# Performance work log

Hardware: AMD Instinct MI355X
Metric: run time of the kernel (lower is better)

## Reference

```python
import jax, jax.numpy as jnp
import numpy as np

HEADS = 8
DK = 64            # key_size == size_per_head
NEIGHBORS = 3
KSIZE = 1 + 2 * NEIGHBORS  # 7 (rate=1)


def setup_inputs() -> dict:
    key = jax.random.key(0)
    k1, k2, k3, k4 = jax.random.split(key, 4)
    B, HW, S, D = 2, 64, 256, 512
    inputs = jax.random.normal(k1, (B, HW, S, D), dtype=jnp.float32)
    pos_bias = jax.random.normal(k2, (HEADS, S, KSIZE), dtype=jnp.float32)
    W_qkv = jax.random.normal(k3, (D, 3 * HEADS * DK), dtype=jnp.float32) * 0.02
    W_out = jax.random.normal(k4, (HEADS * DK, D), dtype=jnp.float32) * 0.02
    return {"inputs": inputs, "pos_bias": pos_bias, "W_qkv": W_qkv, "W_out": W_out}


def reference(inputs, pos_bias, W_qkv, W_out):
    B, HW, S, D = inputs.shape
    # qkv projection (no bias), split into q, k, v
    qkv = inputs @ W_qkv                                   # [B,HW,S,3*H*DK]
    q, k, v = jnp.split(qkv, 3, axis=-1)
    q = (q / jnp.sqrt(jnp.float32(DK))).reshape(B, HW, S, HEADS, DK)
    k = k.reshape(B, HW, S, HEADS, DK)
    v = v.reshape(B, HW, S, HEADS, DK)

    # zero-pad keys/values along seq (faithful to F.pad with value=0)
    pad = NEIGHBORS
    kp = jnp.pad(k, ((0, 0), (0, 0), (pad, pad), (0, 0), (0, 0)))
    vp = jnp.pad(v, ((0, 0), (0, 0), (pad, pad), (0, 0), (0, 0)))

    # sliding-window gather: window w for query i covers padded positions i..i+KSIZE-1
    idx = jnp.arange(S)[:, None] + jnp.arange(KSIZE)[None, :]  # [S,KSIZE]
    kw = kp[:, :, idx]                                         # [B,HW,S,KSIZE,H,DK]
    vw = vp[:, :, idx]                                         # [B,HW,S,KSIZE,H,DK]

    # scores over the window
    attn = jnp.einsum('bnshd,bnswhd->bnswh', q, kw)            # [B,HW,S,KSIZE,H]
    # additive positional bias: [H,S,KSIZE] -> [S,KSIZE,H] broadcast
    attn = attn + jnp.transpose(pos_bias, (1, 2, 0))[None, None]
    attn = jax.nn.softmax(attn, axis=-2)                       # softmax over window dim

    out = jnp.einsum('bnswh,bnswhd->bnshd', attn, vw)          # [B,HW,S,H,DK]
    out = out.reshape(B, HW, S, HEADS * DK)
    return out @ W_out
```

## Files before the change

kernel.cpp:

```cpp
#include <hip/hip_runtime.h>
#include <hip/hip_bf16.h>
#include <cstdint>


typedef __bf16 bf16x8 __attribute__((ext_vector_type(8)));
typedef float f32x4 __attribute__((ext_vector_type(4)));

__device__ __forceinline__ uint16_t f2bf(float f) {
    uint32_t u = __builtin_bit_cast(uint32_t, f);
    return (uint16_t)((u + 0x7fffu + ((u >> 16) & 1u)) >> 16);
}
__device__ __forceinline__ float bflo(uint32_t u) { return __builtin_bit_cast(float, u << 16); }
__device__ __forceinline__ float bfhi(uint32_t u) { return __builtin_bit_cast(float, u & 0xffff0000u); }

__device__ __forceinline__ void unpack8(uint4 v, float* f) {
    f[0] = bflo(v.x); f[1] = bfhi(v.x);
    f[2] = bflo(v.y); f[3] = bfhi(v.y);
    f[4] = bflo(v.z); f[5] = bfhi(v.z);
    f[6] = bflo(v.w); f[7] = bfhi(v.w);
}
__device__ __forceinline__ uint32_t pack2(float a, float b) {
    return (uint32_t)f2bf(a) | ((uint32_t)f2bf(b) << 16);
}

#define GLOAD_LDS16(gp, lp)                                                        \
    __builtin_amdgcn_global_load_lds((const __attribute__((address_space(1))) void*)(gp), \
                                     (__attribute__((address_space(3))) void*)(lp), 16, 0, 0)

__device__ __forceinline__ bf16x8 ds_read16(const uint16_t* p) {
    bf16x8 r;
    asm volatile("ds_read_b128 %0, %1"
                 : "=v"(r)
                 : "v"((const __attribute__((address_space(3))) void*)p));
    return r;
}

__global__ void cvt_f32_bf16(const float* __restrict__ in, uint16_t* __restrict__ out, int n8) {
    int i = blockIdx.x * 256 + threadIdx.x;
    if (i >= n8) return;
    const float4* p = (const float4*)in + (size_t)i * 2;
    float4 a = p[0], b = p[1];
    uint4 o;
    o.x = pack2(a.x, a.y);
    o.y = pack2(a.z, a.w);
    o.z = pack2(b.x, b.y);
    o.w = pack2(b.z, b.w);
    *((uint4*)out + i) = o;
}

__global__ void transpose_cvt(const float* __restrict__ in, uint16_t* __restrict__ out,
                              int R, int C) {
    int idx = blockIdx.x * 256 + threadIdx.x;
    if (idx >= R * C) return;
    int r = idx / C;
    int c = idx - r * C;
    out[(size_t)c * R + r] = f2bf(in[idx]);
}

template <bool F32OUT>
__global__ __launch_bounds__(512, 2)
void gemm256(const uint16_t* __restrict__ A, const uint16_t* __restrict__ BT,
             void* __restrict__ Cout, int M, int N, int K) {
    __shared__ __align__(16) uint16_t lds[65536];

    const int tid  = threadIdx.x;
    const int lane = tid & 63;
    const int wv   = tid >> 6;
    const int r    = lane & 15;
    const int quad = lane >> 4;
    const int wr   = wv >> 2;
    const int wc   = wv & 3;
    const long bm0 = (long)blockIdx.x * 256;
    const long bn0 = (long)blockIdx.y * 256;
    const int NT   = K >> 6;

    const int c0 = tid, c1 = tid + 512;
    const int row0 = c0 >> 3, row1 = c1 >> 3;
    const int sw0 = ((c0 & 7) ^ (row0 & 7)) * 8;
    const int sw1 = ((c1 & 7) ^ (row1 & 7)) * 8;
    const uint16_t* pA0 = A  + (bm0 + row0) * (long)K + sw0;
    const uint16_t* pA1 = A  + (bm0 + row1) * (long)K + sw1;
    const uint16_t* pB0 = BT + (bn0 + row0) * (long)K + sw0;
    const uint16_t* pB1 = BT + (bn0 + row1) * (long)K + sw1;
    const long hstep = 128 * (long)K;

#define STAGE_A(b_, h_, t_) do {                                                        \
        GLOAD_LDS16(pA0 + (h_) * hstep + (t_) * 64,                                     \
                    &lds[(b_) * 16384 + (h_) * 8192 + c0 * 8]);                         \
        GLOAD_LDS16(pA1 + (h_) * hstep + (t_) * 64,                                     \
                    &lds[(b_) * 16384 + (h_) * 8192 + c1 * 8]);                         \
    } while (0)
#define STAGE_B(b_, h_, t_) do {                                                        \
        GLOAD_LDS16(pB0 + (h_) * hstep + (t_) * 64,                                     \
                    &lds[32768 + (b_) * 16384 + (h_) * 8192 + c0 * 8]);                 \
        GLOAD_LDS16(pB1 + (h_) * hstep + (t_) * 64,                                     \
                    &lds[32768 + (b_) * 16384 + (h_) * 8192 + c1 * 8]);                 \
    } while (0)

    const int swk0 = ((0 + quad) ^ (r & 7)) * 8;
    const int swk1 = ((4 + quad) ^ (r & 7)) * 8;
    const int arow = (wr * 128 + r) * 64;
    const int brow = (wc * 64 + r) * 64;

#define DS_A(mf_, kk_) ds_read16(&lds[aoff + arow + (mf_) * 1024 + ((kk_) ? swk1 : swk0)])
#define DS_B(nf_, kk_) ds_read16(&lds[boff + brow + (nf_) * 1024 + ((kk_) ? swk1 : swk0)])

    f32x4 acc[8][4];
#pragma unroll
    for (int mf = 0; mf < 8; ++mf)
#pragma unroll
        for (int nf = 0; nf < 4; ++nf) acc[mf][nf] = (f32x4){0.f, 0.f, 0.f, 0.f};

    STAGE_A(0, 0, 0); STAGE_A(0, 1, 0);
    STAGE_B(0, 0, 0); STAGE_B(0, 1, 0);
    STAGE_B(1, 0, 1); STAGE_B(1, 1, 1);
    asm volatile("s_waitcnt vmcnt(4)" ::: "memory");
    __builtin_amdgcn_s_barrier();

#define MFMA_PHASE(mbase_)                                                              \
    __builtin_amdgcn_s_barrier();                                                       \
    asm volatile("s_waitcnt lgkmcnt(0)" ::: "memory");                                  \
    __builtin_amdgcn_sched_barrier(0);                                                  \
    __builtin_amdgcn_s_setprio(1);                                                      \
    _Pragma("unroll")                                                                   \
    for (int kk = 0; kk < 2; ++kk)                                                      \
        _Pragma("unroll")                                                               \
        for (int mi = 0; mi < 2; ++mi)                                                  \
            _Pragma("unroll")                                                           \
            for (int nf = 0; nf < 4; ++nf)                                              \
                acc[(mbase_) + mi][nf] = __builtin_amdgcn_mfma_f32_16x16x32_bf16(       \
                    af[mi][kk], bfr[nf][kk], acc[(mbase_) + mi][nf], 0, 0, 0);          \
    __builtin_amdgcn_s_setprio(0);

    for (int t = 0; t < NT; ++t) {
        const int b    = t & 1;
        const int aoff = b * 16384;
        const int boff = 32768 + b * 16384;

        bf16x8 bfr[4][2];
        bf16x8 af[2][2];

#pragma unroll
        for (int nf = 0; nf < 4; ++nf) { bfr[nf][0] = DS_B(nf, 0); bfr[nf][1] = DS_B(nf, 1); }
        af[0][0] = DS_A(0, 0); af[0][1] = DS_A(0, 1);
        af[1][0] = DS_A(1, 0); af[1][1] = DS_A(1, 1);
        if (t + 1 < NT) STAGE_A(b ^ 1, 0, t + 1);
        MFMA_PHASE(0)
        __builtin_amdgcn_s_barrier();

        af[0][0] = DS_A(2, 0); af[0][1] = DS_A(2, 1);
        af[1][0] = DS_A(3, 0); af[1][1] = DS_A(3, 1);
        if (t + 1 < NT) STAGE_A(b ^ 1, 1, t + 1);
        MFMA_PHASE(2)
        __builtin_amdgcn_s_barrier();

        af[0][0] = DS_A(4, 0); af[0][1] = DS_A(4, 1);
        af[1][0] = DS_A(5, 0); af[1][1] = DS_A(5, 1);
        if (t + 2 < NT) STAGE_B(b, 0, t + 2);
        MFMA_PHASE(4)
        __builtin_amdgcn_s_barrier();

        af[0][0] = DS_A(6, 0); af[0][1] = DS_A(6, 1);
        af[1][0] = DS_A(7, 0); af[1][1] = DS_A(7, 1);
        if (t + 2 < NT) STAGE_B(b, 1, t + 2);
        MFMA_PHASE(6)
        if (t + 1 < NT) {
            if (t + 2 < NT) asm volatile("s_waitcnt vmcnt(4)" ::: "memory");
            else            asm volatile("s_waitcnt vmcnt(0)" ::: "memory");
            __builtin_amdgcn_s_barrier();
        }
    }

#pragma unroll
    for (int mf = 0; mf < 8; ++mf) {
#pragma unroll
        for (int i = 0; i < 4; ++i) {
            long m = bm0 + wr * 128 + mf * 16 + quad * 4 + i;
            if (F32OUT) {
                float* crow = (float*)Cout + m * (long)N + bn0 + wc * 64 + r;
#pragma unroll
                for (int nf = 0; nf < 4; ++nf) crow[nf * 16] = acc[mf][nf][i];
            } else {
                uint16_t* crow = (uint16_t*)Cout + m * (long)N + bn0 + wc * 64 + r;
#pragma unroll
                for (int nf = 0; nf < 4; ++nf) crow[nf * 16] = f2bf(acc[mf][nf][i]);
            }
        }
    }
#undef STAGE_A
#undef STAGE_B
#undef DS_A
#undef DS_B
#undef MFMA_PHASE
}

__global__ __launch_bounds__(256, 2)
void local_attn(const uint16_t* __restrict__ qkv, const float* __restrict__ pb,
                uint16_t* __restrict__ attn) {
    __shared__ uint4 smem[4096];

    const int h  = blockIdx.x & 7;
    const int bn = blockIdx.x >> 3;
    const int s  = threadIdx.x;
    const size_t base = (size_t)bn * 256 * 1536;

#pragma unroll
    for (int it = 0; it < 16; ++it) {
        int i   = threadIdx.x + it * 256;
        int a   = i >> 11;
        int idx = i & 2047;
        int sp  = idx >> 3;
        int c8  = idx & 7;
        const uint16_t* src = qkv + base + (size_t)sp * 1536 + 512 + a * 512 + h * 64 + c8 * 8;
        smem[a * 2048 + sp * 8 + (c8 ^ (sp & 7))] = *(const uint4*)src;
    }

    const uint16_t* qrow = qkv + base + (size_t)s * 1536 + h * 64;
    uint4 qc[8];
#pragma unroll
    for (int c = 0; c < 8; ++c) qc[c] = *(const uint4*)(qrow + c * 8);

    __syncthreads();

    float sc[7];
#pragma unroll
    for (int w = 0; w < 7; ++w) sc[w] = 0.f;

#pragma unroll
    for (int c = 0; c < 8; ++c) {
        float qf[8];
        unpack8(qc[c], qf);
#pragma unroll
        for (int w = 0; w < 7; ++w) {
            int sp = s + w - 3;
            if ((unsigned)sp < 256u) {
                uint4 kc = smem[sp * 8 + (c ^ (sp & 7))];
                float kf[8];
                unpack8(kc, kf);
#pragma unroll
                for (int j = 0; j < 8; ++j) sc[w] += qf[j] * kf[j];
            }
        }
    }

    const float* pbr = pb + ((size_t)h * 256 + s) * 7;
    float mx = -1e30f;
#pragma unroll
    for (int w = 0; w < 7; ++w) {
        sc[w] = sc[w] * 0.125f + pbr[w];
        mx = fmaxf(mx, sc[w]);
    }
    float p[7], sum = 0.f;
#pragma unroll
    for (int w = 0; w < 7; ++w) {
        p[w] = __expf(sc[w] - mx);
        sum += p[w];
    }
    const float inv = 1.f / sum;
#pragma unroll
    for (int w = 0; w < 7; ++w) p[w] *= inv;

    uint4 ov[8];
#pragma unroll
    for (int c = 0; c < 8; ++c) {
        float o[8] = {0.f, 0.f, 0.f, 0.f, 0.f, 0.f, 0.f, 0.f};
#pragma unroll
        for (int w = 0; w < 7; ++w) {
            int sp = s + w - 3;
            if ((unsigned)sp < 256u) {
                uint4 vc = smem[2048 + sp * 8 + (c ^ (sp & 7))];
                float vf[8];
                unpack8(vc, vf);
#pragma unroll
                for (int j = 0; j < 8; ++j) o[j] += p[w] * vf[j];
            }
        }
        ov[c].x = pack2(o[0], o[1]);
        ov[c].y = pack2(o[2], o[3]);
        ov[c].z = pack2(o[4], o[5]);
        ov[c].w = pack2(o[6], o[7]);
    }

    uint16_t* orow = attn + ((size_t)(bn * 256 + s)) * 512 + h * 64;
#pragma unroll
    for (int c = 0; c < 8; ++c) *(uint4*)(orow + c * 8) = ov[c];
}

extern "C" void kernel_launch(void* const* d_in, const int* in_sizes, int n_in,
                              void* d_out, int out_size, void* d_ws, size_t ws_size,
                              hipStream_t stream) {
    const float* X    = (const float*)d_in[0];
    const float* pb   = (const float*)d_in[1];
    const float* Wqkv = (const float*)d_in[2];
    const float* Wout = (const float*)d_in[3];
    float* out = (float*)d_out;

    char* ws = (char*)d_ws;
    uint16_t* WqkvT = (uint16_t*)(ws);
    uint16_t* WoutT = (uint16_t*)(ws + 1572864);
    uint16_t* qkvb  = (uint16_t*)(ws + 2097152);
    uint16_t* Xb    = (uint16_t*)(ws + 102760448);
    uint16_t* attnb = Xb;

    cvt_f32_bf16<<<(32768 * 512 / 8 + 255) / 256, 256, 0, stream>>>(X, Xb, 32768 * 512 / 8);
    transpose_cvt<<<(512 * 1536 + 255) / 256, 256, 0, stream>>>(Wqkv, WqkvT, 512, 1536);
    transpose_cvt<<<(512 * 512 + 255) / 256, 256, 0, stream>>>(Wout, WoutT, 512, 512);

    gemm256<false><<<dim3(128, 6), 512, 0, stream>>>(Xb, WqkvT, qkvb, 32768, 1536, 512);
    local_attn<<<1024, 256, 0, stream>>>(qkvb, pb, attnb);
    gemm256<true><<<dim3(128, 2), 512, 0, stream>>>(attnb, WoutT, out, 32768, 512, 512);
}
```

Baseline: 258.2 us.

## Restructure GEMM main loop to double-buffer A fragments with partial LDS waits

Rewrites the GEMM inner loop so that A-fragment LDS reads for the next MFMA cluster are issued into a second register set while the current cluster runs, using lgkmcnt(4) partial waits. The four per-phase block barriers are dropped. A and B tiles for step t+1 are now prefetched together into the other buffer, replacing the old schedule where B ran two steps ahead. The aim is to cut barrier stalls and hide LDS latency behind MFMAs. The cost is more VGPRs, a full vmcnt(0) wait each iteration, and less global-load lookahead.

```diff
diff --git a/kernel.cpp b/kernel.cpp
--- a/kernel.cpp
+++ b/kernel.cpp
@@ -105,22 +105,12 @@
 #define DS_A(mf_, kk_) ds_read16(&lds[aoff + arow + (mf_) * 1024 + ((kk_) ? swk1 : swk0)])
 #define DS_B(nf_, kk_) ds_read16(&lds[boff + brow + (nf_) * 1024 + ((kk_) ? swk1 : swk0)])
 
-    f32x4 acc[8][4];
-#pragma unroll
-    for (int mf = 0; mf < 8; ++mf)
-#pragma unroll
-        for (int nf = 0; nf < 4; ++nf) acc[mf][nf] = (f32x4){0.f, 0.f, 0.f, 0.f};
-
-    STAGE_A(0, 0, 0); STAGE_A(0, 1, 0);
-    STAGE_B(0, 0, 0); STAGE_B(0, 1, 0);
-    STAGE_B(1, 0, 1); STAGE_B(1, 1, 1);
-    asm volatile("s_waitcnt vmcnt(4)" ::: "memory");
-    __builtin_amdgcn_s_barrier();
-
-#define MFMA_PHASE(mbase_)                                                              \
-    __builtin_amdgcn_s_barrier();                                                       \
-    asm volatile("s_waitcnt lgkmcnt(0)" ::: "memory");                                  \
-    __builtin_amdgcn_sched_barrier(0);                                                  \
+#define WAITK4 do { asm volatile("s_waitcnt lgkmcnt(4)" ::: "memory");                  \
+                    __builtin_amdgcn_sched_barrier(0); } while (0)
+#define WAITK0 do { asm volatile("s_waitcnt lgkmcnt(0)" ::: "memory");                  \
+                    __builtin_amdgcn_sched_barrier(0); } while (0)
+
+#define MFMA_CL(mbase_, ar_)                                                            \
     __builtin_amdgcn_s_setprio(1);                                                      \
     _Pragma("unroll")                                                                   \
     for (int kk = 0; kk < 2; ++kk)                                                      \
@@ -129,44 +119,57 @@
             _Pragma("unroll")                                                           \
             for (int nf = 0; nf < 4; ++nf)                                              \
                 acc[(mbase_) + mi][nf] = __builtin_amdgcn_mfma_f32_16x16x32_bf16(       \
-                    af[mi][kk], bfr[nf][kk], acc[(mbase_) + mi][nf], 0, 0, 0);          \
+                    ar_[mi][kk], bfr[nf][kk], acc[(mbase_) + mi][nf], 0, 0, 0);         \
     __builtin_amdgcn_s_setprio(0);
+
+    f32x4 acc[8][4];
+#pragma unroll
+    for (int mf = 0; mf < 8; ++mf)
+#pragma unroll
+        for (int nf = 0; nf < 4; ++nf) acc[mf][nf] = (f32x4){0.f, 0.f, 0.f, 0.f};
+
+    STAGE_A(0, 0, 0); STAGE_A(0, 1, 0);
+    STAGE_B(0, 0, 0); STAGE_B(0, 1, 0);
+    asm volatile("s_waitcnt vmcnt(0)" ::: "memory");
+    __builtin_amdgcn_s_barrier();
 
     for (int t = 0; t < NT; ++t) {
         const int b    = t & 1;
         const int aoff = b * 16384;
         const int boff = 32768 + b * 16384;
+        const bool pf  = (t + 1 < NT);
 
         bf16x8 bfr[4][2];
-        bf16x8 af[2][2];
+        bf16x8 a0[2][2], a1[2][2];
 
 #pragma unroll
         for (int nf = 0; nf < 4; ++nf) { bfr[nf][0] = DS_B(nf, 0); bfr[nf][1] = DS_B(nf, 1); }
-        af[0][0] = DS_A(0, 0); af[0][1] = DS_A(0, 1);
-        af[1][0] = DS_A(1, 0); af[1][1] = DS_A(1, 1);
-        if (t + 1 < NT) STAGE_A(b ^ 1, 0, t + 1);
-        MFMA_PHASE(0)
-        __builtin_amdgcn_s_barrier();
-
-        af[0][0] = DS_A(2, 0); af[0][1] = DS_A(2, 1);
-        af[1][0] = DS_A(3, 0); af[1][1] = DS_A(3, 1);
-        if (t + 1 < NT) STAGE_A(b ^ 1, 1, t + 1);
-        MFMA_PHASE(2)
-        __builtin_amdgcn_s_barrier();
-
-        af[0][0] = DS_A(4, 0); af[0][1] = DS_A(4, 1);
-        af[1][0] = DS_A(5, 0); af[1][1] = DS_A(5, 1);
-        if (t + 2 < NT) STAGE_B(b, 0, t + 2);
-        MFMA_PHASE(4)
-        __builtin_amdgcn_s_barrier();
-
-        af[0][0] = DS_A(6, 0); af[0][1] = DS_A(6, 1);
-        af[1][0] = DS_A(7, 0); af[1][1] = DS_A(7, 1);
-        if (t + 2 < NT) STAGE_B(b, 1, t + 2);
-        MFMA_PHASE(6)
-        if (t + 1 < NT) {
-            if (t + 2 < NT) asm volatile("s_waitcnt vmcnt(4)" ::: "memory");
-            else            asm volatile("s_waitcnt vmcnt(0)" ::: "memory");
+        a0[0][0] = DS_A(0, 0); a0[0][1] = DS_A(0, 1);
+        a0[1][0] = DS_A(1, 0); a0[1][1] = DS_A(1, 1);
+        if (pf) { STAGE_A(b ^ 1, 0, t + 1); STAGE_B(b ^ 1, 0, t + 1); }
+
+        a1[0][0] = DS_A(2, 0); a1[0][1] = DS_A(2, 1);
+        a1[1][0] = DS_A(3, 0); a1[1][1] = DS_A(3, 1);
+        if (pf) { STAGE_A(b ^ 1, 1, t + 1); STAGE_B(b ^ 1, 1, t + 1); }
+
+        WAITK4;
+        MFMA_CL(0, a0)
+
+        a0[0][0] = DS_A(4, 0); a0[0][1] = DS_A(4, 1);
+        a0[1][0] = DS_A(5, 0); a0[1][1] = DS_A(5, 1);
+        WAITK4;
+        MFMA_CL(2, a1)
+
+        a1[0][0] = DS_A(6, 0); a1[0][1] = DS_A(6, 1);
+        a1[1][0] = DS_A(7, 0); a1[1][1] = DS_A(7, 1);
+        WAITK4;
+        MFMA_CL(4, a0)
+
+        WAITK0;
+        MFMA_CL(6, a1)
+
+        if (pf) {
+            asm volatile("s_waitcnt vmcnt(0)" ::: "memory");
             __builtin_amdgcn_s_barrier();
         }
     }
@@ -191,7 +194,9 @@
 #undef STAGE_B
 #undef DS_A
 #undef DS_B
-#undef MFMA_PHASE
+#undef WAITK4
+#undef WAITK0
+#undef MFMA_CL
 }
 
 __global__ __launch_bounds__(256, 2)
```

After: 251.8 us. 1.03x faster.
